# Kernel optimization log

Hardware: AMD Instinct MI355X
Metric: run time of the kernel (lower is better)

## Reference

```python
import jax, jax.numpy as jnp
import numpy as np

B, C, H, W = 32, 256, 56, 56   # batch, in_channels, spatial
OC, R, K = 256, 64, 3          # out_channels, low rank, kernel size
PAD, STRIDE = 1, 1


def setup_inputs() -> dict:
    key = jax.random.key(0)
    kx, ku, kv = jax.random.split(key, 3)
    x = jax.random.normal(kx, (B, C, H, W), dtype=jnp.float32)
    # Per-offset low-rank factors: U[i,j] is (out_c, r), V[i,j] is (r, in_c),
    # matching nn.ParameterDict of 1x1 conv weights in the torch module.
    U = jax.random.normal(ku, (K, K, OC, R), dtype=jnp.float32) * 0.05
    V = jax.random.normal(kv, (K, K, R, C), dtype=jnp.float32) * 0.05
    return {"x": x, "U": U, "V": V}


def reference(x, U, V):
    k = U.shape[0]
    pad, stride = PAD, STRIDE
    b, c, h_in, w_in = x.shape
    h_out = (h_in + 2 * pad - (k - 1) - 1) // stride + 1
    w_out = (w_in + 2 * pad - (k - 1) - 1) // stride + 1
    xp = jnp.pad(x, ((0, 0), (0, 0), (pad, pad), (pad, pad)))
    total = jnp.zeros((b, U.shape[2], h_out, w_out), dtype=x.dtype)
    # Loop over the k*k fixed spatial offsets (structurally distinct params),
    # using strided views instead of materializing the unfolded tensor.
    for i in range(k):
        for j in range(k):
            sl = xp[:, :, i:i + (h_out - 1) * stride + 1:stride,
                          j:j + (w_out - 1) * stride + 1:stride]  # [b,c,ho,wo]
            t = jnp.einsum('bchw,rc->brhw', sl, V[i, j])          # V 1x1 conv
            total = total + jnp.einsum('brhw,or->bohw', t, U[i, j])  # U 1x1 conv
    return total
```

## Files before the change

kernel.cpp:

```cpp
#include <hip/hip_runtime.h>
#include <hip/hip_bf16.h>
#include <stdint.h>
#include <stddef.h>

typedef __hip_bfloat16 bf16;
typedef __attribute__((ext_vector_type(8))) short bf16x8;
typedef __attribute__((ext_vector_type(4))) float f32x4;

namespace {
constexpr int kB = 32, kC = 256, kH = 56, kW = 56, kOC = 256, kR = 64;
constexpr int kHP = 58, kWP = 58;
constexpr int kPlane = kH * kW;
constexpr int kNPix  = kB * kPlane;
constexpr int kBM = 128, kBN = 128, kBK = 32;
constexpr int kKSteps = 9 * (kC / kBK);
}

__device__ __forceinline__ void gload16(const void* g, void* lds_wave_uniform) {
    __builtin_amdgcn_global_load_lds(
        (const __attribute__((address_space(1))) uint32_t*)(uintptr_t)g,
        (__attribute__((address_space(3))) uint32_t*)(uint32_t)(uintptr_t)lds_wave_uniform,
        16, 0, 0);
}

__device__ __forceinline__ unsigned short f2bf(float f) {
    union { float f; unsigned int u; } cv; cv.f = f;
    const unsigned int u = cv.u;
    return (unsigned short)((u + 0x7FFFu + ((u >> 16) & 1u)) >> 16);
}

__global__ void merge_weights(const float* __restrict__ U, const float* __restrict__ V,
                              bf16* __restrict__ Wb) {
    const int tap = blockIdx.x >> 8;
    const int o   = blockIdx.x & 255;
    const int c   = threadIdx.x;
    const float* u = U + (size_t)(tap * kOC + o) * kR;
    const float* v = V + (size_t)(tap * kR) * kC + c;
    float acc = 0.f;
#pragma unroll
    for (int r = 0; r < kR; ++r) acc += u[r] * v[r * kC];
    Wb[(size_t)(tap * kOC + o) * kC + c] = __float2bfloat16(acc);
}

__global__ __launch_bounds__(256)
void pad_nhwc(const float* __restrict__ x, bf16* __restrict__ xt) {
    const int b  = blockIdx.x / kHP;
    const int hp = blockIdx.x % kHP;
    const int tid = threadIdx.x;
    bf16* dst = xt + (size_t)(b * kHP + hp) * (kWP * kC);

    if (hp == 0 || hp == kHP - 1) {
        uint4* d4 = (uint4*)dst;
        constexpr int n16 = (kWP * kC * 2) / 16;
        for (int i = tid; i < n16; i += 256) d4[i] = uint4{0, 0, 0, 0};
        return;
    }

    const int h = hp - 1;
    __shared__ unsigned short t[256][58];

    const int w4 = tid & 15;
    const int cb = tid >> 4;
#pragma unroll
    for (int pass = 0; pass < 16; ++pass) {
        const int c = pass * 16 + cb;
        if (w4 < 14) {
            const float4 v = *reinterpret_cast<const float4*>(
                x + ((size_t)(b * kC + c) * kH + h) * kW + w4 * 4);
            t[c][w4 * 4 + 0] = f2bf(v.x);
            t[c][w4 * 4 + 1] = f2bf(v.y);
            t[c][w4 * 4 + 2] = f2bf(v.z);
            t[c][w4 * 4 + 3] = f2bf(v.w);
        }
    }
    __syncthreads();

    const int c2   = (tid & 127) * 2;
    const int half = tid >> 7;
    unsigned int* dw = (unsigned int*)dst;
#pragma unroll
    for (int wpi = 0; wpi < 29; ++wpi) {
        const int wp = wpi * 2 + half;
        unsigned int val = 0;
        if (wp >= 1 && wp <= kW) {
            const int w = wp - 1;
            val = (unsigned int)t[c2][w] | ((unsigned int)t[c2 + 1][w] << 16);
        }
        dw[(size_t)wp * 128 + (c2 >> 1)] = val;
    }
}

__global__ __launch_bounds__(256, 4)
void conv_mfma(const bf16* __restrict__ Wb, const bf16* __restrict__ xt,
               float* __restrict__ out) {
    __shared__ bf16 Asm[2][kBM * kBK];
    __shared__ bf16 Bsm[2][kBM * kBK];

    const int tid  = threadIdx.x;
    const int lane = tid & 63;
    const int wid  = tid >> 6;

    const int bid = blockIdx.x;
    constexpr int cpx = (kNPix / kBN) * (kOC / kBM) / 8;
    const int swz = (bid & 7) * cpx + (bid >> 3);
    const int ocb = (swz & 1) * kBM;
    const int p0  = (swz >> 1) * kBN;

    const int rowL = lane >> 2;
    const int row1 = wid * 32 + rowL;
    const int sw   = (lane >> 3) & 3;
    const int coff = (((lane & 3) ^ sw)) * 8;

    const bf16* gA1 = Wb + (size_t)(ocb + row1) * kC + coff;

    const int gp1 = p0 + row1;
    const int gp2 = gp1 + 16;
    const int b1 = gp1 / kPlane, q1 = gp1 - b1 * kPlane;
    const int b2 = gp2 / kPlane, q2 = gp2 - b2 * kPlane;
    const int h1 = q1 / kW, w1 = q1 - h1 * kW;
    const int h2 = q2 / kW, w2 = q2 - h2 * kW;
    const bf16* gB1 = xt + ((size_t)((b1 * kHP + h1) * kWP + w1)) * kC + coff;
    const bf16* gB2 = xt + ((size_t)((b2 * kHP + h2) * kWP + w2)) * kC + coff;

    const int wr = wid >> 1, wc = wid & 1;
    const int lrow = lane & 15;
    const int rcs  = (((lane >> 4) ^ ((lrow >> 1) & 3))) * 8;

    f32x4 acc[4][4] = {};

    auto stage = [&](int buf, int ks) {
        const int tap  = ks >> 3;
        const int c0   = (ks & 7) * kBK;
        const int aoff = tap * (kOC * kC) + c0;
        const int boff = ((tap / 3) * kWP + (tap % 3)) * kC + c0;
        char* AsmB = (char*)(&Asm[buf][0]) + wid * 2048;
        char* BsmB = (char*)(&Bsm[buf][0]) + wid * 2048;
        gload16(gA1 + aoff,           AsmB);
        gload16(gA1 + aoff + 16 * kC, AsmB + 1024);
        gload16(gB1 + boff,           BsmB);
        gload16(gB2 + boff,           BsmB + 1024);
    };

    stage(0, 0);
    asm volatile("s_waitcnt vmcnt(0)\ns_barrier" ::: "memory");

    int cur = 0;
    for (int ks = 0; ks < kKSteps; ++ks) {
        if (ks + 1 < kKSteps) stage(cur ^ 1, ks + 1);

        const bf16* Acur = &Asm[cur][0];
        const bf16* Bcur = &Bsm[cur][0];
        bf16x8 af[4], bfr[4];
#pragma unroll
        for (int mi = 0; mi < 4; ++mi)
            af[mi] = *(const bf16x8*)&Acur[(wr * 64 + mi * 16 + lrow) * kBK + rcs];
#pragma unroll
        for (int nj = 0; nj < 4; ++nj)
            bfr[nj] = *(const bf16x8*)&Bcur[(wc * 64 + nj * 16 + lrow) * kBK + rcs];
#pragma unroll
        for (int mi = 0; mi < 4; ++mi)
#pragma unroll
            for (int nj = 0; nj < 4; ++nj)
                acc[mi][nj] = __builtin_amdgcn_mfma_f32_16x16x32_bf16(
                    af[mi], bfr[nj], acc[mi][nj], 0, 0, 0);

        asm volatile("s_waitcnt vmcnt(0)\ns_barrier" ::: "memory");
        cur ^= 1;
    }

#pragma unroll
    for (int nj = 0; nj < 4; ++nj) {
        const int gp = p0 + wc * 64 + nj * 16 + lrow;
        const int bb = gp / kPlane;
        const int qq = gp - bb * kPlane;
        float* ob = out + (size_t)bb * (kOC * kPlane) + qq;
#pragma unroll
        for (int mi = 0; mi < 4; ++mi) {
            const int o = ocb + wr * 64 + mi * 16 + (lane >> 4) * 4;
            float* op = ob + (size_t)o * kPlane;
#pragma unroll
            for (int r = 0; r < 4; ++r)
                op[(size_t)r * kPlane] = acc[mi][nj][r];
        }
    }
}

extern "C" void kernel_launch(void* const* d_in, const int* in_sizes, int n_in,
                              void* d_out, int out_size, void* d_ws, size_t ws_size,
                              hipStream_t stream) {
    const float* x = (const float*)d_in[0];
    const float* U = (const float*)d_in[1];
    const float* V = (const float*)d_in[2];
    float* out = (float*)d_out;

    bf16* Wb = (bf16*)d_ws;
    bf16* xt = (bf16*)((char*)d_ws + (size_t)9 * kOC * kC * 2);

    merge_weights<<<dim3(9 * kOC), dim3(kC), 0, stream>>>(U, V, Wb);
    pad_nhwc<<<dim3(kB * kHP), dim3(256), 0, stream>>>(x, xt);
    conv_mfma<<<dim3(kNPix / kBN * (kOC / kBM)), dim3(256), 0, stream>>>(Wb, xt, out);
}
```

Baseline: 344.1 us.

## Enlarge conv GEMM tile to 256x256x64 with 512-thread workgroups

```diff
diff --git a/kernel.cpp b/kernel.cpp
--- a/kernel.cpp
+++ b/kernel.cpp
@@ -12,8 +12,10 @@
 constexpr int kHP = 58, kWP = 58;
 constexpr int kPlane = kH * kW;
 constexpr int kNPix  = kB * kPlane;
-constexpr int kBM = 128, kBN = 128, kBK = 32;
-constexpr int kKSteps = 9 * (kC / kBK);
+constexpr int kBM = 256, kBN = 256, kBK = 64;
+constexpr int kKT = 9 * (kC / kBK);
+constexpr int kAT = kBM * kBK;
+constexpr int kBTile = kBN * kBK;
 }
 
 __device__ __forceinline__ void gload16(const void* g, void* lds_wave_uniform) {
@@ -90,97 +92,119 @@
     }
 }
 
-__global__ __launch_bounds__(256, 4)
+__global__ __launch_bounds__(512, 1)
 void conv_mfma(const bf16* __restrict__ Wb, const bf16* __restrict__ xt,
                float* __restrict__ out) {
-    __shared__ bf16 Asm[2][kBM * kBK];
-    __shared__ bf16 Bsm[2][kBM * kBK];
+    __shared__ bf16 Asm[2 * kAT];
+    __shared__ bf16 Bsm[2 * kBTile];
 
     const int tid  = threadIdx.x;
     const int lane = tid & 63;
     const int wid  = tid >> 6;
 
+    constexpr int nwg = kNPix / kBN;
+    constexpr int cpx = nwg / 8;
     const int bid = blockIdx.x;
-    constexpr int cpx = (kNPix / kBN) * (kOC / kBM) / 8;
     const int swz = (bid & 7) * cpx + (bid >> 3);
-    const int ocb = (swz & 1) * kBM;
-    const int p0  = (swz >> 1) * kBN;
-
-    const int rowL = lane >> 2;
-    const int row1 = wid * 32 + rowL;
-    const int sw   = (lane >> 3) & 3;
-    const int coff = (((lane & 3) ^ sw)) * 8;
-
-    const bf16* gA1 = Wb + (size_t)(ocb + row1) * kC + coff;
-
-    const int gp1 = p0 + row1;
-    const int gp2 = gp1 + 16;
-    const int b1 = gp1 / kPlane, q1 = gp1 - b1 * kPlane;
-    const int b2 = gp2 / kPlane, q2 = gp2 - b2 * kPlane;
-    const int h1 = q1 / kW, w1 = q1 - h1 * kW;
-    const int h2 = q2 / kW, w2 = q2 - h2 * kW;
-    const bf16* gB1 = xt + ((size_t)((b1 * kHP + h1) * kWP + w1)) * kC + coff;
-    const bf16* gB2 = xt + ((size_t)((b2 * kHP + h2) * kWP + w2)) * kC + coff;
-
-    const int wr = wid >> 1, wc = wid & 1;
+    const int p0  = swz * kBN;
+
+    const int l3 = lane >> 3;
+    const int l7 = lane & 7;
+    const int skoff = (l7 ^ l3) * 8;
+
+    const bf16* gA[4];
+#pragma unroll
+    for (int i = 0; i < 4; ++i)
+        gA[i] = Wb + (size_t)(wid * 32 + i * 8 + l3) * kC + skoff;
+
+    const bf16* gB[4];
+#pragma unroll
+    for (int i = 0; i < 4; ++i) {
+        const int gp = p0 + wid * 32 + i * 8 + l3;
+        const int bb = gp / kPlane, q = gp - bb * kPlane;
+        const int hh = q / kW, ww = q - hh * kW;
+        gB[i] = xt + ((size_t)((bb * kHP + hh) * kWP + ww)) * kC + skoff;
+    }
+
+    auto stage = [&](int t, int buf) {
+        const int tap = t >> 2;
+        const int c0  = (t & 3) * kBK;
+        const size_t aoff = (size_t)tap * (kOC * kC) + c0;
+        const size_t boff = (size_t)((tap / 3) * kWP + (tap % 3)) * kC + c0;
+        char* Ad = (char*)(Asm + buf * kAT) + wid * 4096;
+        char* Bd = (char*)(Bsm + buf * kBTile) + wid * 4096;
+#pragma unroll
+        for (int i = 0; i < 4; ++i) gload16(gA[i] + aoff, Ad + i * 1024);
+#pragma unroll
+        for (int i = 0; i < 4; ++i) gload16(gB[i] + boff, Bd + i * 1024);
+    };
+
+    const int wr   = wid >> 2;
+    const int wcn  = wid & 3;
     const int lrow = lane & 15;
-    const int rcs  = (((lane >> 4) ^ ((lrow >> 1) & 3))) * 8;
-
-    f32x4 acc[4][4] = {};
-
-    auto stage = [&](int buf, int ks) {
-        const int tap  = ks >> 3;
-        const int c0   = (ks & 7) * kBK;
-        const int aoff = tap * (kOC * kC) + c0;
-        const int boff = ((tap / 3) * kWP + (tap % 3)) * kC + c0;
-        char* AsmB = (char*)(&Asm[buf][0]) + wid * 2048;
-        char* BsmB = (char*)(&Bsm[buf][0]) + wid * 2048;
-        gload16(gA1 + aoff,           AsmB);
-        gload16(gA1 + aoff + 16 * kC, AsmB + 1024);
-        gload16(gB1 + boff,           BsmB);
-        gload16(gB2 + boff,           BsmB + 1024);
-    };
+    const int qt   = lane >> 4;
+    const int ck[2] = { (qt ^ (lrow & 7)) * 8, ((4 | qt) ^ (lrow & 7)) * 8 };
+
+    f32x4 acc[8][4] = {};
 
     stage(0, 0);
-    asm volatile("s_waitcnt vmcnt(0)\ns_barrier" ::: "memory");
-
-    int cur = 0;
-    for (int ks = 0; ks < kKSteps; ++ks) {
-        if (ks + 1 < kKSteps) stage(cur ^ 1, ks + 1);
-
-        const bf16* Acur = &Asm[cur][0];
-        const bf16* Bcur = &Bsm[cur][0];
-        bf16x8 af[4], bfr[4];
-#pragma unroll
-        for (int mi = 0; mi < 4; ++mi)
-            af[mi] = *(const bf16x8*)&Acur[(wr * 64 + mi * 16 + lrow) * kBK + rcs];
+    for (int t = 0; t < kKT; ++t) {
+        const int buf = t & 1;
+        if (t + 1 < kKT) {
+            stage(t + 1, buf ^ 1);
+            asm volatile("s_waitcnt vmcnt(8)" ::: "memory");
+        } else {
+            asm volatile("s_waitcnt vmcnt(0)" ::: "memory");
+        }
+        __builtin_amdgcn_s_barrier();
+
+        const bf16* Ac = Asm + buf * kAT;
+        const bf16* Bc = Bsm + buf * kBTile;
+
+        bf16x8 bfr[4][2];
 #pragma unroll
         for (int nj = 0; nj < 4; ++nj)
-            bfr[nj] = *(const bf16x8*)&Bcur[(wc * 64 + nj * 16 + lrow) * kBK + rcs];
-#pragma unroll
-        for (int mi = 0; mi < 4; ++mi)
-#pragma unroll
-            for (int nj = 0; nj < 4; ++nj)
-                acc[mi][nj] = __builtin_amdgcn_mfma_f32_16x16x32_bf16(
-                    af[mi], bfr[nj], acc[mi][nj], 0, 0, 0);
-
-        asm volatile("s_waitcnt vmcnt(0)\ns_barrier" ::: "memory");
-        cur ^= 1;
+#pragma unroll
+            for (int ko = 0; ko < 2; ++ko)
+                bfr[nj][ko] = *(const bf16x8*)(Bc + (wcn * 64 + nj * 16 + lrow) * kBK + ck[ko]);
+
+#pragma unroll
+        for (int mh = 0; mh < 2; ++mh) {
+            bf16x8 af[4][2];
+#pragma unroll
+            for (int mi = 0; mi < 4; ++mi)
+#pragma unroll
+                for (int ko = 0; ko < 2; ++ko)
+                    af[mi][ko] = *(const bf16x8*)(Ac + (wr * 128 + mh * 64 + mi * 16 + lrow) * kBK + ck[ko]);
+            __builtin_amdgcn_s_setprio(1);
+#pragma unroll
+            for (int mi = 0; mi < 4; ++mi)
+#pragma unroll
+                for (int nj = 0; nj < 4; ++nj)
+#pragma unroll
+                    for (int ko = 0; ko < 2; ++ko)
+                        acc[mh * 4 + mi][nj] = __builtin_amdgcn_mfma_f32_16x16x32_bf16(
+                            af[mi][ko], bfr[nj][ko], acc[mh * 4 + mi][nj], 0, 0, 0);
+            __builtin_amdgcn_s_setprio(0);
+        }
+
+        asm volatile("s_waitcnt lgkmcnt(0)" ::: "memory");
+        __builtin_amdgcn_s_barrier();
     }
 
 #pragma unroll
     for (int nj = 0; nj < 4; ++nj) {
-        const int gp = p0 + wc * 64 + nj * 16 + lrow;
+        const int gp = p0 + wcn * 64 + nj * 16 + lrow;
         const int bb = gp / kPlane;
         const int qq = gp - bb * kPlane;
         float* ob = out + (size_t)bb * (kOC * kPlane) + qq;
 #pragma unroll
-        for (int mi = 0; mi < 4; ++mi) {
-            const int o = ocb + wr * 64 + mi * 16 + (lane >> 4) * 4;
+        for (int mi8 = 0; mi8 < 8; ++mi8) {
+            const int o = wr * 128 + mi8 * 16 + qt * 4;
             float* op = ob + (size_t)o * kPlane;
 #pragma unroll
             for (int r = 0; r < 4; ++r)
-                op[(size_t)r * kPlane] = acc[mi][nj][r];
+                op[(size_t)r * kPlane] = acc[mi8][nj][r];
         }
     }
 }
@@ -198,5 +222,5 @@
 
     merge_weights<<<dim3(9 * kOC), dim3(kC), 0, stream>>>(U, V, Wb);
     pad_nhwc<<<dim3(kB * kHP), dim3(256), 0, stream>>>(x, xt);
-    conv_mfma<<<dim3(kNPix / kBN * (kOC / kBM)), dim3(256), 0, stream>>>(Wb, xt, out);
-}
+    conv_mfma<<<dim3(kNPix / kBN), dim3(512), 0, stream>>>(Wb, xt, out);
+}
```

Measured after the change: 346.8 us. Within noise of the previous version (+0.8%).
